# Kernel tuning notes

Measured on AMD Instinct MI355X. Metric: run time of the kernel, lower is better.

## Reference

```python
import jax, jax.numpy as jnp
import numpy as np

EPS = 1e-8  # torch.cosine_similarity eps


def setup_inputs() -> dict:
    key = jax.random.key(0)
    ks = jax.random.split(key, 6)
    B, D, R, T = 131072, 512, 128, 3
    return {
        "x_encoded": jax.random.normal(ks[0], (B, D), dtype=jnp.float32),
        "register": jax.random.normal(ks[1], (R, D), dtype=jnp.float32),
        "W": jax.random.normal(ks[2], (D, D), dtype=jnp.float32) / np.sqrt(D),
        "b": jax.random.normal(ks[3], (D,), dtype=jnp.float32) * 0.01,
        "low_rank_u": jax.random.normal(ks[4], (T,), dtype=jnp.float32),
        "low_rank_v": jax.random.normal(ks[5], (D,), dtype=jnp.float32),
        "k": 3,
    }


def reference(x_encoded, register, W, b, low_rank_u, low_rank_v, k):
    # mode='finetune' path of TSRegister.get_register_tokens
    # data_projection: Linear(d_model, d_model)
    xe = x_encoded @ W.T + b                      # [B, D]
    # cosine similarity vs codebook: dot / max(|x||r|, eps)
    xn = jnp.linalg.norm(xe, axis=-1)             # [B]
    rn = jnp.linalg.norm(register, axis=-1)       # [R]
    sims = (xe @ register.T) / jnp.maximum(xn[:, None] * rn[None, :], EPS)  # [B, R]
    top_k_values, top_k_indices = jax.lax.top_k(sims, k)  # [B, k]
    selected_centers = register[top_k_indices]    # gather -> [B, k, D]
    adaptation_matrix = jnp.outer(low_rank_u, low_rank_v)  # [k, D] (k == num_register_tokens)
    adapted_centers = selected_centers + adaptation_matrix[None, :, :]
    return adapted_centers, top_k_indices, top_k_values
```

## Files before the change

kernel.cpp:

```cpp
#include <hip/hip_runtime.h>

#define TSTR 68
#define XESTR 68
#define SSTR 129

__device__ __forceinline__ unsigned long long pack_key(float s, int col) {
    unsigned u = __float_as_uint(s);
    unsigned m = (u & 0x80000000u) ? ~u : (u | 0x80000000u);
    return ((unsigned long long)m << 32) | (unsigned)(127 - col);
}
__device__ __forceinline__ float key_val(unsigned long long k) {
    unsigned m = (unsigned)(k >> 32);
    unsigned u = (m & 0x80000000u) ? (m ^ 0x80000000u) : ~m;
    return __uint_as_float(u);
}
__device__ __forceinline__ int key_col(unsigned long long k) {
    return 127 - (int)(k & 0xFFFFFFFFu);
}
__device__ __forceinline__ void ins3(unsigned long long x,
        unsigned long long &a0, unsigned long long &a1, unsigned long long &a2) {
    if (x > a0)      { a2 = a1; a1 = a0; a0 = x; }
    else if (x > a1) { a2 = a1; a1 = x; }
    else if (x > a2) { a2 = x; }
}

__global__ void rn_kernel(const float* __restrict__ cb, float* __restrict__ rn) {
    const int j = blockIdx.x;
    const int t = threadIdx.x;
    double a = 0.0;
#pragma unroll
    for (int m = 0; m < 8; ++m) {
        float f = cb[j * 512 + m * 64 + t];
        a += (double)f * (double)f;
    }
#pragma unroll
    for (int off = 32; off >= 1; off >>= 1)
        a += __shfl_down(a, off);
    if (t == 0) rn[j] = (float)sqrt(a);
}

__global__ __launch_bounds__(256, 3) void fused_kernel(
    const float* __restrict__ x, const float* __restrict__ cb,
    const float* __restrict__ W, const float* __restrict__ bias,
    const float* __restrict__ u, const float* __restrict__ v,
    const float* __restrict__ rn, float* __restrict__ out,
    size_t idx_off, size_t val_off)
{
    __shared__ __align__(16) float uA[128 * TSTR];
    __shared__ __align__(16) float xeL[64 * XESTR];
    __shared__ float rnL[128];
    __shared__ float xnL[64];
    __shared__ unsigned char idxL[64 * 3];

    const int tid = threadIdx.x;
    const int tlo = tid & 15;
    const int thi = tid >> 4;
    const int row0 = blockIdx.x << 6;

    if (tid < 128) rnL[tid] = rn[tid];

    const int srow = tid >> 2;
    const int scol = (tid & 3) << 4;

    float m2[4][8];
#pragma unroll
    for (int i = 0; i < 4; ++i)
#pragma unroll
        for (int j = 0; j < 8; ++j) m2[i][j] = 0.f;
    float nacc = 0.f;

    for (int dc = 0; dc < 8; ++dc) {
        float m1[4][4];
#pragma unroll
        for (int i = 0; i < 4; ++i)
#pragma unroll
            for (int j = 0; j < 4; ++j) m1[i][j] = 0.f;

        for (int kc = 0; kc < 8; ++kc) {
            __syncthreads();
            {
                const float4* gx = (const float4*)(x + (size_t)(row0 + srow) * 512 + kc * 64 + scol);
                const float4* gw = (const float4*)(W + (size_t)(dc * 64 + srow) * 512 + kc * 64 + scol);
                float4* dx = (float4*)&uA[srow * TSTR + scol];
                float4* dw = (float4*)&uA[64 * TSTR + srow * TSTR + scol];
#pragma unroll
                for (int m = 0; m < 4; ++m) { dx[m] = gx[m]; dw[m] = gw[m]; }
            }
            __syncthreads();
            float s1[4][4];
#pragma unroll
            for (int i = 0; i < 4; ++i)
#pragma unroll
                for (int j = 0; j < 4; ++j) s1[i][j] = 0.f;
#pragma unroll
            for (int kk = 0; kk < 16; ++kk) {
                float4 xa[4], wa[4];
#pragma unroll
                for (int i = 0; i < 4; ++i)
                    xa[i] = *(const float4*)&uA[(thi + 16 * i) * TSTR + (kk << 2)];
#pragma unroll
                for (int j = 0; j < 4; ++j)
                    wa[j] = *(const float4*)&uA[64 * TSTR + (tlo + 16 * j) * TSTR + (kk << 2)];
#pragma unroll
                for (int i = 0; i < 4; ++i)
#pragma unroll
                    for (int j = 0; j < 4; ++j) {
                        s1[i][j] = fmaf(xa[i].x, wa[j].x, s1[i][j]);
                        s1[i][j] = fmaf(xa[i].y, wa[j].y, s1[i][j]);
                        s1[i][j] = fmaf(xa[i].z, wa[j].z, s1[i][j]);
                        s1[i][j] = fmaf(xa[i].w, wa[j].w, s1[i][j]);
                    }
            }
#pragma unroll
            for (int i = 0; i < 4; ++i)
#pragma unroll
                for (int j = 0; j < 4; ++j) m1[i][j] += s1[i][j];
        }
#pragma unroll
        for (int j = 0; j < 4; ++j) {
            float bj = bias[dc * 64 + tlo + 16 * j];
#pragma unroll
            for (int i = 0; i < 4; ++i)
                xeL[(thi + 16 * i) * XESTR + tlo + 16 * j] = m1[i][j] + bj;
        }
        __syncthreads();
        {
            const float4* gr = (const float4*)(cb + (size_t)(tid >> 1) * 512 + dc * 64 + ((tid & 1) << 5));
            float4* dr = (float4*)&uA[(tid >> 1) * TSTR + ((tid & 1) << 5)];
#pragma unroll
            for (int m = 0; m < 8; ++m) dr[m] = gr[m];
        }
        if (tid < 64) {
#pragma unroll
            for (int dd = 0; dd < 16; ++dd) {
                float4 q = *(const float4*)&xeL[tid * XESTR + (dd << 2)];
                nacc = fmaf(q.x, q.x, nacc);
                nacc = fmaf(q.y, q.y, nacc);
                nacc = fmaf(q.z, q.z, nacc);
                nacc = fmaf(q.w, q.w, nacc);
            }
        }
        __syncthreads();
        float s2[4][8];
#pragma unroll
        for (int i = 0; i < 4; ++i)
#pragma unroll
            for (int j = 0; j < 8; ++j) s2[i][j] = 0.f;
#pragma unroll
        for (int dd = 0; dd < 16; ++dd) {
            float4 xv[4], rv[8];
#pragma unroll
            for (int i = 0; i < 4; ++i)
                xv[i] = *(const float4*)&xeL[(tlo + 16 * i) * XESTR + (dd << 2)];
#pragma unroll
            for (int j = 0; j < 8; ++j)
                rv[j] = *(const float4*)&uA[(thi + 16 * j) * TSTR + (dd << 2)];
#pragma unroll
            for (int i = 0; i < 4; ++i)
#pragma unroll
                for (int j = 0; j < 8; ++j) {
                    s2[i][j] = fmaf(xv[i].x, rv[j].x, s2[i][j]);
                    s2[i][j] = fmaf(xv[i].y, rv[j].y, s2[i][j]);
                    s2[i][j] = fmaf(xv[i].z, rv[j].z, s2[i][j]);
                    s2[i][j] = fmaf(xv[i].w, rv[j].w, s2[i][j]);
                }
        }
#pragma unroll
        for (int i = 0; i < 4; ++i)
#pragma unroll
            for (int j = 0; j < 8; ++j) m2[i][j] += s2[i][j];
    }
    __syncthreads();
#pragma unroll
    for (int i = 0; i < 4; ++i)
#pragma unroll
        for (int j = 0; j < 8; ++j)
            uA[(tlo + 16 * i) * SSTR + thi + 16 * j] = m2[i][j];
    if (tid < 64) xnL[tid] = sqrtf(nacc);
    __syncthreads();

    {
        const int row = tid >> 2;
        const int p   = tid & 3;
        const float xn = xnL[row];
        unsigned long long a0 = 0, a1 = 0, a2 = 0;
#pragma unroll
        for (int t = 0; t < 32; ++t) {
            const int c = p + 4 * t;
            float s = uA[row * SSTR + c] / fmaxf(xn * rnL[c], 1e-8f);
            ins3(pack_key(s, c), a0, a1, a2);
        }
#pragma unroll
        for (int mask = 1; mask <= 2; mask <<= 1) {
            unsigned long long b0 = __shfl_xor(a0, mask);
            unsigned long long b1 = __shfl_xor(a1, mask);
            unsigned long long b2 = __shfl_xor(a2, mask);
            ins3(b0, a0, a1, a2); ins3(b1, a0, a1, a2); ins3(b2, a0, a1, a2);
        }
        if (p == 0) {
            const size_t g = (size_t)(row0 + row);
            float* oi = out + idx_off + g * 3;
            float* ov = out + val_off + g * 3;
            oi[0] = (float)key_col(a0); oi[1] = (float)key_col(a1); oi[2] = (float)key_col(a2);
            ov[0] = key_val(a0); ov[1] = key_val(a1); ov[2] = key_val(a2);
            idxL[row * 3 + 0] = (unsigned char)key_col(a0);
            idxL[row * 3 + 1] = (unsigned char)key_col(a1);
            idxL[row * 3 + 2] = (unsigned char)key_col(a2);
        }
    }
    __syncthreads();

    const float uu0 = u[0], uu1 = u[1], uu2 = u[2];
#pragma unroll
    for (int q = 0; q < 3; ++q) {
        int task = tid + 256 * q;
        int row = task / 12;
        int rem = task - row * 12;
        int tt  = rem >> 2;
        int seg = rem & 3;
        int idx = idxL[row * 3 + tt];
        float uu = (tt == 0) ? uu0 : ((tt == 1) ? uu1 : uu2);
        const float4* gr4 = (const float4*)(cb + (size_t)idx * 512 + seg * 128);
        const float4* gv4 = (const float4*)(v + seg * 128);
        float4* ob = (float4*)(out + ((size_t)(row0 + row) * 3 + tt) * 512 + seg * 128);
#pragma unroll
        for (int c2 = 0; c2 < 32; ++c2) {
            float4 rv = gr4[c2];
            float4 vv = gv4[c2];
            float4 o;
            o.x = fmaf(uu, vv.x, rv.x);
            o.y = fmaf(uu, vv.y, rv.y);
            o.z = fmaf(uu, vv.z, rv.z);
            o.w = fmaf(uu, vv.w, rv.w);
            ob[c2] = o;
        }
    }
}

extern "C" void kernel_launch(void* const* d_in, const int* in_sizes, int n_in,
                              void* d_out, int out_size, void* d_ws, size_t ws_size,
                              hipStream_t stream) {
    const float* x  = (const float*)d_in[0];
    const float* cb = (const float*)d_in[1];
    const float* W  = (const float*)d_in[2];
    const float* b  = (const float*)d_in[3];
    const float* u  = (const float*)d_in[4];
    const float* v  = (const float*)d_in[5];
    float* rn = (float*)d_ws;
    float* out = (float*)d_out;

    const size_t B = (size_t)in_sizes[0] / 512;
    const size_t val_off = (size_t)out_size - 3 * B;
    const size_t idx_off = (size_t)out_size - 6 * B;

    hipLaunchKernelGGL(rn_kernel, dim3(128), dim3(64), 0, stream, cb, rn);
    hipLaunchKernelGGL(fused_kernel, dim3((unsigned)(B / 64)), dim3(256), 0, stream,
                       x, cb, W, b, u, v, rn, out, idx_off, val_off);
}
```

Baseline: 1.644 ms.

## Software-prefetch next x/W/codebook tiles into registers to overlap global loads

Global loads for the next K-chunk of x and W, and for the codebook slice, are now issued into registers right after the shared-memory barrier, so they run while the current tile's FMAs execute. Stores to shared memory then read from those registers instead of waiting on global memory. This is meant to hide global load latency behind compute. The cost is 64 extra VGPRs per thread for the prefetch buffers, which may lower occupancy.

```diff
diff --git a/kernel.cpp b/kernel.cpp
--- a/kernel.cpp
+++ b/kernel.cpp
@@ -62,12 +62,25 @@
     const int srow = tid >> 2;
     const int scol = (tid & 3) << 4;
 
+    const float* gx0  = x  + (size_t)(row0 + srow) * 512 + scol;
+    const float* gw0  = W  + (size_t)srow * 512 + scol;
+    const float* gcb0 = cb + (size_t)(tid >> 1) * 512 + ((tid & 1) << 5);
+
+    float4 px[4], pw[4], pcb[8];
+
     float m2[4][8];
 #pragma unroll
     for (int i = 0; i < 4; ++i)
 #pragma unroll
         for (int j = 0; j < 8; ++j) m2[i][j] = 0.f;
     float nacc = 0.f;
+
+    {
+        const float4* gx = (const float4*)(gx0);
+        const float4* gw = (const float4*)(gw0);
+#pragma unroll
+        for (int m = 0; m < 4; ++m) { px[m] = gx[m]; pw[m] = gw[m]; }
+    }
 
     for (int dc = 0; dc < 8; ++dc) {
         float m1[4][4];
@@ -79,14 +92,22 @@
         for (int kc = 0; kc < 8; ++kc) {
             __syncthreads();
             {
-                const float4* gx = (const float4*)(x + (size_t)(row0 + srow) * 512 + kc * 64 + scol);
-                const float4* gw = (const float4*)(W + (size_t)(dc * 64 + srow) * 512 + kc * 64 + scol);
                 float4* dx = (float4*)&uA[srow * TSTR + scol];
                 float4* dw = (float4*)&uA[64 * TSTR + srow * TSTR + scol];
 #pragma unroll
-                for (int m = 0; m < 4; ++m) { dx[m] = gx[m]; dw[m] = gw[m]; }
+                for (int m = 0; m < 4; ++m) { dx[m] = px[m]; dw[m] = pw[m]; }
             }
             __syncthreads();
+            if (kc < 7) {
+                const float4* gx = (const float4*)(gx0 + (kc + 1) * 64);
+                const float4* gw = (const float4*)(gw0 + (size_t)dc * 32768 + (kc + 1) * 64);
+#pragma unroll
+                for (int m = 0; m < 4; ++m) { px[m] = gx[m]; pw[m] = gw[m]; }
+            } else {
+                const float4* gr = (const float4*)(gcb0 + dc * 64);
+#pragma unroll
+                for (int m = 0; m < 8; ++m) pcb[m] = gr[m];
+            }
             float s1[4][4];
 #pragma unroll
             for (int i = 0; i < 4; ++i)
@@ -125,10 +146,9 @@
         }
         __syncthreads();
         {
-            const float4* gr = (const float4*)(cb + (size_t)(tid >> 1) * 512 + dc * 64 + ((tid & 1) << 5));
             float4* dr = (float4*)&uA[(tid >> 1) * TSTR + ((tid & 1) << 5)];
 #pragma unroll
-            for (int m = 0; m < 8; ++m) dr[m] = gr[m];
+            for (int m = 0; m < 8; ++m) dr[m] = pcb[m];
         }
         if (tid < 64) {
 #pragma unroll
@@ -141,6 +161,12 @@
             }
         }
         __syncthreads();
+        if (dc < 7) {
+            const float4* gx = (const float4*)(gx0);
+            const float4* gw = (const float4*)(gw0 + (size_t)(dc + 1) * 32768);
+#pragma unroll
+            for (int m = 0; m < 4; ++m) { px[m] = gx[m]; pw[m] = gw[m]; }
+        }
         float s2[4][8];
 #pragma unroll
         for (int i = 0; i < 4; ++i)
```

After: 2.506 ms. 52.4% more time.

## Split fused kernel into 128x128-tiled projection GEMM and similarity/top-k kernel

Applied to the files above, without the earlier changes.

The fused per-64-row kernel becomes two kernels. The first computes the projection xe with 128x128 tiles and 8x8 register blocking, with global loads staged through registers, and writes xe as scratch into the output buffer at a row stride of 1536. The second reads xe back with a 128-row tile to compute norms, codebook similarities, top-3 and the gather. The aim is higher arithmetic intensity and fewer barriers per FMA, paid for with an extra global round trip of xe and higher register pressure (occupancy hint lowered from 3 to 2). Scratch in the output buffer is overwritten later by the adapted-centers writes, which depends on the ordering between the two kernels.

```diff
diff --git a/kernel.cpp b/kernel.cpp
--- a/kernel.cpp
+++ b/kernel.cpp
@@ -1,7 +1,6 @@
 #include <hip/hip_runtime.h>
 
-#define TSTR 68
-#define XESTR 68
+#define ASTR 68
 #define SSTR 129
 
 __device__ __forceinline__ unsigned long long pack_key(float s, int col) {
@@ -39,124 +38,156 @@
     if (t == 0) rn[j] = (float)sqrt(a);
 }
 
-__global__ __launch_bounds__(256, 3) void fused_kernel(
-    const float* __restrict__ x, const float* __restrict__ cb,
-    const float* __restrict__ W, const float* __restrict__ bias,
-    const float* __restrict__ u, const float* __restrict__ v,
-    const float* __restrict__ rn, float* __restrict__ out,
-    size_t idx_off, size_t val_off)
+__global__ __launch_bounds__(256, 2) void xe_kernel(
+    const float* __restrict__ x, const float* __restrict__ W,
+    const float* __restrict__ bias, float* xe)
 {
-    __shared__ __align__(16) float uA[128 * TSTR];
-    __shared__ __align__(16) float xeL[64 * XESTR];
+    __shared__ __align__(16) float xT[128 * ASTR];
+    __shared__ __align__(16) float wT[128 * ASTR];
+
+    const int tid  = threadIdx.x;
+    const int rowg = tid >> 4;
+    const int colg = tid & 15;
+    const int row0 = blockIdx.x << 7;
+    const int col0 = blockIdx.y << 7;
+
+    const int sr = tid >> 1;
+    const int sc = (tid & 1) << 5;
+    const float* gx0 = x + (size_t)(row0 + sr) * 512 + sc;
+    const float* gw0 = W + (size_t)(col0 + sr) * 512 + sc;
+    float4* dx = (float4*)&xT[sr * ASTR + sc];
+    float4* dw = (float4*)&wT[sr * ASTR + sc];
+
+    float m1[8][8];
+#pragma unroll
+    for (int i = 0; i < 8; ++i)
+#pragma unroll
+        for (int j = 0; j < 8; ++j) m1[i][j] = 0.f;
+
+    for (int kc = 0; kc < 8; ++kc) {
+        float4 rx[8], rw[8];
+        {
+            const float4* gx = (const float4*)(gx0 + kc * 64);
+            const float4* gw = (const float4*)(gw0 + kc * 64);
+#pragma unroll
+            for (int m = 0; m < 8; ++m) { rx[m] = gx[m]; rw[m] = gw[m]; }
+        }
+        __syncthreads();
+#pragma unroll
+        for (int m = 0; m < 8; ++m) { dx[m] = rx[m]; dw[m] = rw[m]; }
+        __syncthreads();
+
+        float s1[8][8];
+#pragma unroll
+        for (int i = 0; i < 8; ++i)
+#pragma unroll
+            for (int j = 0; j < 8; ++j) s1[i][j] = 0.f;
+#pragma unroll
+        for (int kk = 0; kk < 16; ++kk) {
+            float4 xa[8], wa[8];
+#pragma unroll
+            for (int i = 0; i < 8; ++i)
+                xa[i] = *(const float4*)&xT[(rowg + 16 * i) * ASTR + (kk << 2)];
+#pragma unroll
+            for (int j = 0; j < 8; ++j)
+                wa[j] = *(const float4*)&wT[(colg + 16 * j) * ASTR + (kk << 2)];
+#pragma unroll
+            for (int i = 0; i < 8; ++i)
+#pragma unroll
+                for (int j = 0; j < 8; ++j) {
+                    s1[i][j] = fmaf(xa[i].x, wa[j].x, s1[i][j]);
+                    s1[i][j] = fmaf(xa[i].y, wa[j].y, s1[i][j]);
+                    s1[i][j] = fmaf(xa[i].z, wa[j].z, s1[i][j]);
+                    s1[i][j] = fmaf(xa[i].w, wa[j].w, s1[i][j]);
+                }
+        }
+#pragma unroll
+        for (int i = 0; i < 8; ++i)
+#pragma unroll
+            for (int j = 0; j < 8; ++j) m1[i][j] += s1[i][j];
+    }
+#pragma unroll
+    for (int j = 0; j < 8; ++j) {
+        const float bj = bias[col0 + colg + 16 * j];
+#pragma unroll
+        for (int i = 0; i < 8; ++i)
+            xe[(size_t)(row0 + rowg + 16 * i) * 1536 + col0 + colg + 16 * j] = m1[i][j] + bj;
+    }
+}
+
+__global__ __launch_bounds__(256, 2) void sims_kernel(
+    const float* __restrict__ cb, const float* __restrict__ u,
+    const float* __restrict__ v, const float* __restrict__ rn,
+    float* out, size_t idx_off, size_t val_off)
+{
+    __shared__ __align__(16) float shB[2 * 128 * ASTR];
     __shared__ float rnL[128];
-    __shared__ float xnL[64];
-    __shared__ unsigned char idxL[64 * 3];
-
-    const int tid = threadIdx.x;
-    const int tlo = tid & 15;
-    const int thi = tid >> 4;
-    const int row0 = blockIdx.x << 6;
+    __shared__ float xnL[128];
+    __shared__ unsigned char idxL[128 * 3];
+
+    float* eT = shB;
+    float* cT = shB + 128 * ASTR;
+
+    const int tid  = threadIdx.x;
+    const int rowg = tid >> 4;
+    const int colg = tid & 15;
+    const int row0 = blockIdx.x << 7;
 
     if (tid < 128) rnL[tid] = rn[tid];
 
-    const int srow = tid >> 2;
-    const int scol = (tid & 3) << 4;
-
-    float m2[4][8];
-#pragma unroll
-    for (int i = 0; i < 4; ++i)
+    const int sr = tid >> 1;
+    const int sc = (tid & 1) << 5;
+    const float* ge0 = out + (size_t)(row0 + sr) * 1536 + sc;
+    const float* gc0 = cb + (size_t)sr * 512 + sc;
+    float4* de = (float4*)&eT[sr * ASTR + sc];
+    float4* dc = (float4*)&cT[sr * ASTR + sc];
+
+    float m2[8][8];
+#pragma unroll
+    for (int i = 0; i < 8; ++i)
 #pragma unroll
         for (int j = 0; j < 8; ++j) m2[i][j] = 0.f;
     float nacc = 0.f;
 
-    for (int dc = 0; dc < 8; ++dc) {
-        float m1[4][4];
-#pragma unroll
-        for (int i = 0; i < 4; ++i)
-#pragma unroll
-            for (int j = 0; j < 4; ++j) m1[i][j] = 0.f;
-
-        for (int kc = 0; kc < 8; ++kc) {
-            __syncthreads();
-            {
-                const float4* gx = (const float4*)(x + (size_t)(row0 + srow) * 512 + kc * 64 + scol);
-                const float4* gw = (const float4*)(W + (size_t)(dc * 64 + srow) * 512 + kc * 64 + scol);
-                float4* dx = (float4*)&uA[srow * TSTR + scol];
-                float4* dw = (float4*)&uA[64 * TSTR + srow * TSTR + scol];
-#pragma unroll
-                for (int m = 0; m < 4; ++m) { dx[m] = gx[m]; dw[m] = gw[m]; }
-            }
-            __syncthreads();
-            float s1[4][4];
-#pragma unroll
-            for (int i = 0; i < 4; ++i)
-#pragma unroll
-                for (int j = 0; j < 4; ++j) s1[i][j] = 0.f;
-#pragma unroll
-            for (int kk = 0; kk < 16; ++kk) {
-                float4 xa[4], wa[4];
-#pragma unroll
-                for (int i = 0; i < 4; ++i)
-                    xa[i] = *(const float4*)&uA[(thi + 16 * i) * TSTR + (kk << 2)];
-#pragma unroll
-                for (int j = 0; j < 4; ++j)
-                    wa[j] = *(const float4*)&uA[64 * TSTR + (tlo + 16 * j) * TSTR + (kk << 2)];
-#pragma unroll
-                for (int i = 0; i < 4; ++i)
-#pragma unroll
-                    for (int j = 0; j < 4; ++j) {
-                        s1[i][j] = fmaf(xa[i].x, wa[j].x, s1[i][j]);
-                        s1[i][j] = fmaf(xa[i].y, wa[j].y, s1[i][j]);
-                        s1[i][j] = fmaf(xa[i].z, wa[j].z, s1[i][j]);
-                        s1[i][j] = fmaf(xa[i].w, wa[j].w, s1[i][j]);
-                    }
-            }
-#pragma unroll
-            for (int i = 0; i < 4; ++i)
-#pragma unroll
-                for (int j = 0; j < 4; ++j) m1[i][j] += s1[i][j];
-        }
-#pragma unroll
-        for (int j = 0; j < 4; ++j) {
-            float bj = bias[dc * 64 + tlo + 16 * j];
-#pragma unroll
-            for (int i = 0; i < 4; ++i)
-                xeL[(thi + 16 * i) * XESTR + tlo + 16 * j] = m1[i][j] + bj;
-        }
-        __syncthreads();
+    for (int dc2 = 0; dc2 < 8; ++dc2) {
+        float4 re[8], rc[8];
         {
-            const float4* gr = (const float4*)(cb + (size_t)(tid >> 1) * 512 + dc * 64 + ((tid & 1) << 5));
-            float4* dr = (float4*)&uA[(tid >> 1) * TSTR + ((tid & 1) << 5)];
-#pragma unroll
-            for (int m = 0; m < 8; ++m) dr[m] = gr[m];
-        }
-        if (tid < 64) {
+            const float4* ge = (const float4*)(ge0 + dc2 * 64);
+            const float4* gc = (const float4*)(gc0 + dc2 * 64);
+#pragma unroll
+            for (int m = 0; m < 8; ++m) { re[m] = ge[m]; rc[m] = gc[m]; }
+        }
+        __syncthreads();
+#pragma unroll
+        for (int m = 0; m < 8; ++m) { de[m] = re[m]; dc[m] = rc[m]; }
+        __syncthreads();
+
+        if (tid < 128) {
 #pragma unroll
             for (int dd = 0; dd < 16; ++dd) {
-                float4 q = *(const float4*)&xeL[tid * XESTR + (dd << 2)];
+                float4 q = *(const float4*)&eT[tid * ASTR + (dd << 2)];
                 nacc = fmaf(q.x, q.x, nacc);
                 nacc = fmaf(q.y, q.y, nacc);
                 nacc = fmaf(q.z, q.z, nacc);
                 nacc = fmaf(q.w, q.w, nacc);
             }
         }
-        __syncthreads();
-        float s2[4][8];
-#pragma unroll
-        for (int i = 0; i < 4; ++i)
+        float s2[8][8];
+#pragma unroll
+        for (int i = 0; i < 8; ++i)
 #pragma unroll
             for (int j = 0; j < 8; ++j) s2[i][j] = 0.f;
 #pragma unroll
         for (int dd = 0; dd < 16; ++dd) {
-            float4 xv[4], rv[8];
-#pragma unroll
-            for (int i = 0; i < 4; ++i)
-                xv[i] = *(const float4*)&xeL[(tlo + 16 * i) * XESTR + (dd << 2)];
+            float4 xv[8], rv[8];
+#pragma unroll
+            for (int i = 0; i < 8; ++i)
+                xv[i] = *(const float4*)&eT[(rowg + 16 * i) * ASTR + (dd << 2)];
 #pragma unroll
             for (int j = 0; j < 8; ++j)
-                rv[j] = *(const float4*)&uA[(thi + 16 * j) * TSTR + (dd << 2)];
-#pragma unroll
-            for (int i = 0; i < 4; ++i)
+                rv[j] = *(const float4*)&cT[(colg + 16 * j) * ASTR + (dd << 2)];
+#pragma unroll
+            for (int i = 0; i < 8; ++i)
 #pragma unroll
                 for (int j = 0; j < 8; ++j) {
                     s2[i][j] = fmaf(xv[i].x, rv[j].x, s2[i][j]);
@@ -166,35 +197,34 @@
                 }
         }
 #pragma unroll
-        for (int i = 0; i < 4; ++i)
+        for (int i = 0; i < 8; ++i)
 #pragma unroll
             for (int j = 0; j < 8; ++j) m2[i][j] += s2[i][j];
     }
     __syncthreads();
 #pragma unroll
-    for (int i = 0; i < 4; ++i)
+    for (int i = 0; i < 8; ++i)
 #pragma unroll
         for (int j = 0; j < 8; ++j)
-            uA[(tlo + 16 * i) * SSTR + thi + 16 * j] = m2[i][j];
-    if (tid < 64) xnL[tid] = sqrtf(nacc);
+            shB[(rowg + 16 * i) * SSTR + colg + 16 * j] = m2[i][j];
+    if (tid < 128) xnL[tid] = sqrtf(nacc);
     __syncthreads();
 
     {
-        const int row = tid >> 2;
-        const int p   = tid & 3;
+        const int row = tid >> 1;
+        const int p   = tid & 1;
         const float xn = xnL[row];
         unsigned long long a0 = 0, a1 = 0, a2 = 0;
 #pragma unroll
-        for (int t = 0; t < 32; ++t) {
-            const int c = p + 4 * t;
-            float s = uA[row * SSTR + c] / fmaxf(xn * rnL[c], 1e-8f);
+        for (int t = 0; t < 64; ++t) {
+            const int c = p + 2 * t;
+            float s = shB[row * SSTR + c] / fmaxf(xn * rnL[c], 1e-8f);
             ins3(pack_key(s, c), a0, a1, a2);
         }
-#pragma unroll
-        for (int mask = 1; mask <= 2; mask <<= 1) {
-            unsigned long long b0 = __shfl_xor(a0, mask);
-            unsigned long long b1 = __shfl_xor(a1, mask);
-            unsigned long long b2 = __shfl_xor(a2, mask);
+        {
+            unsigned long long b0 = __shfl_xor(a0, 1);
+            unsigned long long b1 = __shfl_xor(a1, 1);
+            unsigned long long b2 = __shfl_xor(a2, 1);
             ins3(b0, a0, a1, a2); ins3(b1, a0, a1, a2); ins3(b2, a0, a1, a2);
         }
         if (p == 0) {
@@ -212,7 +242,7 @@
 
     const float uu0 = u[0], uu1 = u[1], uu2 = u[2];
 #pragma unroll
-    for (int q = 0; q < 3; ++q) {
+    for (int q = 0; q < 6; ++q) {
         int task = tid + 256 * q;
         int row = task / 12;
         int rem = task - row * 12;
@@ -246,7 +276,7 @@
     const float* b  = (const float*)d_in[3];
     const float* u  = (const float*)d_in[4];
     const float* v  = (const float*)d_in[5];
-    float* rn = (float*)d_ws;
+    float* rn  = (float*)d_ws;
     float* out = (float*)d_out;
 
     const size_t B = (size_t)in_sizes[0] / 512;
@@ -254,6 +284,8 @@
     const size_t idx_off = (size_t)out_size - 6 * B;
 
     hipLaunchKernelGGL(rn_kernel, dim3(128), dim3(64), 0, stream, cb, rn);
-    hipLaunchKernelGGL(fused_kernel, dim3((unsigned)(B / 64)), dim3(256), 0, stream,
-                       x, cb, W, b, u, v, rn, out, idx_off, val_off);
-}
+    hipLaunchKernelGGL(xe_kernel, dim3((unsigned)(B / 128), 4), dim3(256), 0, stream,
+                       x, W, b, out);
+    hipLaunchKernelGGL(sims_kernel, dim3((unsigned)(B / 128)), dim3(256), 0, stream,
+                       cb, u, v, rn, out, idx_off, val_off);
+}
```

Measured after the change: 2.894 ms. 1.76x slower.

## Read GEMM operands directly from global memory instead of staging in LDS

Applied to the files above, without the earlier changes.

Removes the shared-memory staging tiles for x, W and the codebook. Each thread now loads its float4 operands straight from global memory (relying on caches), which drops most __syncthreads barriers and frees LDS. Top-3 selection now runs directly on the register accumulators, with per-wave candidates merged through a small LDS buffer, and launch bounds are lowered to 2 blocks per SIMD. The risk is that each global element is now fetched by many threads with strided, uncoalesced patterns, so load traffic and latency may rise sharply.

```diff
diff --git a/kernel.cpp b/kernel.cpp
--- a/kernel.cpp
+++ b/kernel.cpp
@@ -1,8 +1,6 @@
 #include <hip/hip_runtime.h>
 
-#define TSTR 68
 #define XESTR 68
-#define SSTR 129
 
 __device__ __forceinline__ unsigned long long pack_key(float s, int col) {
     unsigned u = __float_as_uint(s);
@@ -39,15 +37,15 @@
     if (t == 0) rn[j] = (float)sqrt(a);
 }
 
-__global__ __launch_bounds__(256, 3) void fused_kernel(
+__global__ __launch_bounds__(256, 2) void fused_kernel(
     const float* __restrict__ x, const float* __restrict__ cb,
     const float* __restrict__ W, const float* __restrict__ bias,
     const float* __restrict__ u, const float* __restrict__ v,
     const float* __restrict__ rn, float* __restrict__ out,
     size_t idx_off, size_t val_off)
 {
-    __shared__ __align__(16) float uA[128 * TSTR];
     __shared__ __align__(16) float xeL[64 * XESTR];
+    __shared__ unsigned long long candL[64 * 12];
     __shared__ float rnL[128];
     __shared__ float xnL[64];
     __shared__ unsigned char idxL[64 * 3];
@@ -55,13 +53,13 @@
     const int tid = threadIdx.x;
     const int tlo = tid & 15;
     const int thi = tid >> 4;
+    const int w   = tid >> 6;
+    const int lane = tid & 63;
     const int row0 = blockIdx.x << 6;
 
     if (tid < 128) rnL[tid] = rn[tid];
 
-    const int srow = tid >> 2;
-    const int scol = (tid & 3) << 4;
-
+    const float* xr0 = x + (size_t)(row0 + thi) * 512;
     float m2[4][8];
 #pragma unroll
     for (int i = 0; i < 4; ++i)
@@ -76,46 +74,39 @@
 #pragma unroll
             for (int j = 0; j < 4; ++j) m1[i][j] = 0.f;
 
+        const float* wr0 = W + (size_t)(dc * 64 + tlo) * 512;
+
         for (int kc = 0; kc < 8; ++kc) {
-            __syncthreads();
-            {
-                const float4* gx = (const float4*)(x + (size_t)(row0 + srow) * 512 + kc * 64 + scol);
-                const float4* gw = (const float4*)(W + (size_t)(dc * 64 + srow) * 512 + kc * 64 + scol);
-                float4* dx = (float4*)&uA[srow * TSTR + scol];
-                float4* dw = (float4*)&uA[64 * TSTR + srow * TSTR + scol];
-#pragma unroll
-                for (int m = 0; m < 4; ++m) { dx[m] = gx[m]; dw[m] = gw[m]; }
+            float s1[4][4];
+#pragma unroll
+            for (int i = 0; i < 4; ++i)
+#pragma unroll
+                for (int j = 0; j < 4; ++j) s1[i][j] = 0.f;
+            const int ko = kc * 64;
+#pragma unroll
+            for (int kk = 0; kk < 16; ++kk) {
+                float4 wa[4];
+#pragma unroll
+                for (int j = 0; j < 4; ++j)
+                    wa[j] = *(const float4*)(wr0 + (size_t)(16 * j) * 512 + ko + (kk << 2));
+#pragma unroll
+                for (int i = 0; i < 4; ++i) {
+                    const float4 xa = *(const float4*)(xr0 + (size_t)(16 * i) * 512 + ko + (kk << 2));
+#pragma unroll
+                    for (int j = 0; j < 4; ++j) {
+                        s1[i][j] = fmaf(xa.x, wa[j].x, s1[i][j]);
+                        s1[i][j] = fmaf(xa.y, wa[j].y, s1[i][j]);
+                        s1[i][j] = fmaf(xa.z, wa[j].z, s1[i][j]);
+                        s1[i][j] = fmaf(xa.w, wa[j].w, s1[i][j]);
+                    }
+                }
             }
-            __syncthreads();
-            float s1[4][4];
-#pragma unroll
-            for (int i = 0; i < 4; ++i)
-#pragma unroll
-                for (int j = 0; j < 4; ++j) s1[i][j] = 0.f;
-#pragma unroll
-            for (int kk = 0; kk < 16; ++kk) {
-                float4 xa[4], wa[4];
-#pragma unroll
-                for (int i = 0; i < 4; ++i)
-                    xa[i] = *(const float4*)&uA[(thi + 16 * i) * TSTR + (kk << 2)];
-#pragma unroll
-                for (int j = 0; j < 4; ++j)
-                    wa[j] = *(const float4*)&uA[64 * TSTR + (tlo + 16 * j) * TSTR + (kk << 2)];
-#pragma unroll
-                for (int i = 0; i < 4; ++i)
-#pragma unroll
-                    for (int j = 0; j < 4; ++j) {
-                        s1[i][j] = fmaf(xa[i].x, wa[j].x, s1[i][j]);
-                        s1[i][j] = fmaf(xa[i].y, wa[j].y, s1[i][j]);
-                        s1[i][j] = fmaf(xa[i].z, wa[j].z, s1[i][j]);
-                        s1[i][j] = fmaf(xa[i].w, wa[j].w, s1[i][j]);
-                    }
-            }
 #pragma unroll
             for (int i = 0; i < 4; ++i)
 #pragma unroll
                 for (int j = 0; j < 4; ++j) m1[i][j] += s1[i][j];
         }
+        __syncthreads();
 #pragma unroll
         for (int j = 0; j < 4; ++j) {
             float bj = bias[dc * 64 + tlo + 16 * j];
@@ -124,12 +115,6 @@
                 xeL[(thi + 16 * i) * XESTR + tlo + 16 * j] = m1[i][j] + bj;
         }
         __syncthreads();
-        {
-            const float4* gr = (const float4*)(cb + (size_t)(tid >> 1) * 512 + dc * 64 + ((tid & 1) << 5));
-            float4* dr = (float4*)&uA[(tid >> 1) * TSTR + ((tid & 1) << 5)];
-#pragma unroll
-            for (int m = 0; m < 8; ++m) dr[m] = gr[m];
-        }
         if (tid < 64) {
 #pragma unroll
             for (int dd = 0; dd < 16; ++dd) {
@@ -140,73 +125,78 @@
                 nacc = fmaf(q.w, q.w, nacc);
             }
         }
-        __syncthreads();
-        float s2[4][8];
-#pragma unroll
-        for (int i = 0; i < 4; ++i)
-#pragma unroll
-            for (int j = 0; j < 8; ++j) s2[i][j] = 0.f;
-#pragma unroll
-        for (int dd = 0; dd < 16; ++dd) {
-            float4 xv[4], rv[8];
-#pragma unroll
-            for (int i = 0; i < 4; ++i)
-                xv[i] = *(const float4*)&xeL[(tlo + 16 * i) * XESTR + (dd << 2)];
-#pragma unroll
-            for (int j = 0; j < 8; ++j)
-                rv[j] = *(const float4*)&uA[(thi + 16 * j) * TSTR + (dd << 2)];
-#pragma unroll
-            for (int i = 0; i < 4; ++i)
-#pragma unroll
-                for (int j = 0; j < 8; ++j) {
-                    s2[i][j] = fmaf(xv[i].x, rv[j].x, s2[i][j]);
-                    s2[i][j] = fmaf(xv[i].y, rv[j].y, s2[i][j]);
-                    s2[i][j] = fmaf(xv[i].z, rv[j].z, s2[i][j]);
-                    s2[i][j] = fmaf(xv[i].w, rv[j].w, s2[i][j]);
+        {
+            const float* cr0 = cb + (size_t)thi * 512 + dc * 64;
+            float s2[4][8];
+#pragma unroll
+            for (int i = 0; i < 4; ++i)
+#pragma unroll
+                for (int j = 0; j < 8; ++j) s2[i][j] = 0.f;
+#pragma unroll
+            for (int dd = 0; dd < 16; ++dd) {
+                float4 rv[8];
+#pragma unroll
+                for (int j = 0; j < 8; ++j)
+                    rv[j] = *(const float4*)(cr0 + (size_t)(16 * j) * 512 + (dd << 2));
+#pragma unroll
+                for (int i = 0; i < 4; ++i) {
+                    const float4 xv = *(const float4*)&xeL[(tlo + 16 * i) * XESTR + (dd << 2)];
+#pragma unroll
+                    for (int j = 0; j < 8; ++j) {
+                        s2[i][j] = fmaf(xv.x, rv[j].x, s2[i][j]);
+                        s2[i][j] = fmaf(xv.y, rv[j].y, s2[i][j]);
+                        s2[i][j] = fmaf(xv.z, rv[j].z, s2[i][j]);
+                        s2[i][j] = fmaf(xv.w, rv[j].w, s2[i][j]);
+                    }
                 }
-        }
-#pragma unroll
-        for (int i = 0; i < 4; ++i)
-#pragma unroll
-            for (int j = 0; j < 8; ++j) m2[i][j] += s2[i][j];
-    }
-    __syncthreads();
-#pragma unroll
-    for (int i = 0; i < 4; ++i)
-#pragma unroll
-        for (int j = 0; j < 8; ++j)
-            uA[(tlo + 16 * i) * SSTR + thi + 16 * j] = m2[i][j];
+            }
+#pragma unroll
+            for (int i = 0; i < 4; ++i)
+#pragma unroll
+                for (int j = 0; j < 8; ++j) m2[i][j] += s2[i][j];
+        }
+    }
     if (tid < 64) xnL[tid] = sqrtf(nacc);
     __syncthreads();
 
-    {
-        const int row = tid >> 2;
-        const int p   = tid & 3;
-        const float xn = xnL[row];
+#pragma unroll
+    for (int i = 0; i < 4; ++i) {
+        const int r = tlo + 16 * i;
+        const float xn = xnL[r];
         unsigned long long a0 = 0, a1 = 0, a2 = 0;
 #pragma unroll
-        for (int t = 0; t < 32; ++t) {
-            const int c = p + 4 * t;
-            float s = uA[row * SSTR + c] / fmaxf(xn * rnL[c], 1e-8f);
+        for (int j = 0; j < 8; ++j) {
+            const int c = thi + 16 * j;
+            float s = m2[i][j] / fmaxf(xn * rnL[c], 1e-8f);
             ins3(pack_key(s, c), a0, a1, a2);
         }
 #pragma unroll
-        for (int mask = 1; mask <= 2; mask <<= 1) {
+        for (int mask = 16; mask <= 32; mask <<= 1) {
             unsigned long long b0 = __shfl_xor(a0, mask);
             unsigned long long b1 = __shfl_xor(a1, mask);
             unsigned long long b2 = __shfl_xor(a2, mask);
             ins3(b0, a0, a1, a2); ins3(b1, a0, a1, a2); ins3(b2, a0, a1, a2);
         }
-        if (p == 0) {
-            const size_t g = (size_t)(row0 + row);
-            float* oi = out + idx_off + g * 3;
-            float* ov = out + val_off + g * 3;
-            oi[0] = (float)key_col(a0); oi[1] = (float)key_col(a1); oi[2] = (float)key_col(a2);
-            ov[0] = key_val(a0); ov[1] = key_val(a1); ov[2] = key_val(a2);
-            idxL[row * 3 + 0] = (unsigned char)key_col(a0);
-            idxL[row * 3 + 1] = (unsigned char)key_col(a1);
-            idxL[row * 3 + 2] = (unsigned char)key_col(a2);
-        }
+        if (lane < 16) {
+            candL[r * 12 + w * 3 + 0] = a0;
+            candL[r * 12 + w * 3 + 1] = a1;
+            candL[r * 12 + w * 3 + 2] = a2;
+        }
+    }
+    __syncthreads();
+
+    if (tid < 64) {
+        unsigned long long a0 = 0, a1 = 0, a2 = 0;
+#pragma unroll
+        for (int m = 0; m < 12; ++m) ins3(candL[tid * 12 + m], a0, a1, a2);
+        const size_t g = (size_t)(row0 + tid);
+        float* oi = out + idx_off + g * 3;
+        float* ov = out + val_off + g * 3;
+        oi[0] = (float)key_col(a0); oi[1] = (float)key_col(a1); oi[2] = (float)key_col(a2);
+        ov[0] = key_val(a0); ov[1] = key_val(a1); ov[2] = key_val(a2);
+        idxL[tid * 3 + 0] = (unsigned char)key_col(a0);
+        idxL[tid * 3 + 1] = (unsigned char)key_col(a1);
+        idxL[tid * 3 + 2] = (unsigned char)key_col(a2);
     }
     __syncthreads();
 
@@ -246,7 +236,7 @@
     const float* b  = (const float*)d_in[3];
     const float* u  = (const float*)d_in[4];
     const float* v  = (const float*)d_in[5];
-    float* rn = (float*)d_ws;
+    float* rn  = (float*)d_ws;
     float* out = (float*)d_out;
 
     const size_t B = (size_t)in_sizes[0] / 512;
```

New measurement: 6.081 ms. 3.7x slower.
